# Performance work log

Hardware: AMD Instinct MI355X
Metric: run time of the kernel (lower is better)

Reference implementation:

```python
import jax, jax.numpy as jnp
import numpy as np
import math

G = 256      # graphs per batch
N0 = 256     # nodes per graph at input
RATIO = 0.5  # TopKPooling ratio


def gcn_conv(x, src, dst, ew, W, b):
    h = x @ W
    n = x.shape[0]
    deg = jnp.zeros((n,), x.dtype).at[dst].add(ew) + 1.0  # +1 for self-loop
    dinv = jax.lax.rsqrt(deg)
    norm = dinv[src] * dinv[dst] * ew
    agg = jnp.zeros_like(h).at[dst].add(norm[:, None] * h[src])
    return agg + h / deg[:, None] + b  # self-loop norm = 1/deg


def topk_pool(x, src, dst, ew, w, n_per_graph):
    # PyG TopKPooling: score = tanh(x.w/||w||); keep top ceil(ratio*n) per graph;
    # x_out = x[perm] * score[perm]; edges between dropped nodes are masked out.
    k = int(math.ceil(RATIO * n_per_graph))
    score = jnp.tanh((x @ w) / jnp.linalg.norm(w))
    top_s, top_i = jax.lax.top_k(score.reshape(G, n_per_graph), k)  # [G,k]
    perm = (top_i + (jnp.arange(G) * n_per_graph)[:, None]).reshape(-1)
    new_x = x[perm] * top_s.reshape(-1, 1)
    new_id = jnp.full((x.shape[0],), -1, jnp.int32).at[perm].set(
        jnp.arange(G * k, dtype=jnp.int32))
    ns, nd = new_id[src], new_id[dst]
    valid = (ns >= 0) & (nd >= 0)
    new_ew = ew * valid.astype(x.dtype)
    ns = jnp.where(valid, ns, 0)
    nd = jnp.where(valid, nd, 0)
    new_batch = jnp.repeat(jnp.arange(G, dtype=jnp.int32), k)
    return new_x, ns, nd, new_ew, new_batch, k


def readout(x, batch):
    # torch.cat([global_max_pool, global_mean_pool], dim=1)
    mx = jax.ops.segment_max(x, batch, num_segments=G)
    cnt = jax.ops.segment_sum(jnp.ones((x.shape[0],), x.dtype), batch, num_segments=G)
    mn = jax.ops.segment_sum(x, batch, num_segments=G) / cnt[:, None]
    return jnp.concatenate([mx, mn], axis=1)


def _forward(x, edge_index, batch, gcn_w0, gcn_b0, gcn_w1, gcn_b1, gcn_w2, gcn_b2,
             pool_w0, pool_w1, pool_w2, lin1_w, lin1_b, lin2_w, lin2_b, lin3_w, lin3_b):
    src, dst = edge_index[0], edge_index[1]
    ew = jnp.ones((src.shape[0],), x.dtype)
    npg = N0
    h = jax.nn.relu(gcn_conv(x, src, dst, ew, gcn_w0, gcn_b0))
    h, src, dst, ew, batch, npg = topk_pool(h, src, dst, ew, pool_w0, npg)
    out = readout(h, batch)
    for Wg, bg, pw in ((gcn_w1, gcn_b1, pool_w1), (gcn_w2, gcn_b2, pool_w2)):
        h = jax.nn.relu(gcn_conv(h, src, dst, ew, Wg, bg))
        h, src, dst, ew, batch, npg = topk_pool(h, src, dst, ew, pw, npg)
        out = out + readout(h, batch)
    h1 = jax.nn.relu(out @ lin1_w + lin1_b)  # dropout = identity (eval mode)
    h2 = jax.nn.relu(h1 @ lin2_w + lin2_b)
    logits = h2 @ lin3_w + lin3_b
    return jax.nn.log_softmax(logits, axis=-1)


def setup_inputs() -> dict:
    key = jax.random.key(0)
    ks = jax.random.split(key, 16)
    EPG = 2048  # edges per graph (avg degree 8)
    F_IN, H = 128, 256
    num_nodes, E = G * N0, G * EPG
    x = jax.random.normal(ks[0], (num_nodes, F_IN), jnp.float32)
    offs = jnp.repeat(jnp.arange(G, dtype=jnp.int32) * N0, EPG)
    src = offs + jax.random.randint(ks[1], (E,), 0, N0, dtype=jnp.int32)
    dst = offs + jax.random.randint(ks[2], (E,), 0, N0, dtype=jnp.int32)

    def glorot(k, shape):
        lim = float(np.sqrt(6.0 / (shape[0] + shape[1])))
        return jax.random.uniform(k, shape, jnp.float32, -lim, lim)

    return {
        "x": x,
        "edge_index": jnp.stack([src, dst]),
        "batch": jnp.arange(num_nodes, dtype=jnp.int32) // N0,
        "gcn_w0": glorot(ks[3], (F_IN, H)), "gcn_b0": jnp.zeros((H,), jnp.float32),
        "gcn_w1": glorot(ks[4], (H, H)), "gcn_b1": jnp.zeros((H,), jnp.float32),
        "gcn_w2": glorot(ks[5], (H, H)), "gcn_b2": jnp.zeros((H,), jnp.float32),
        "pool_w0": jax.random.normal(ks[6], (H,), jnp.float32) * 0.1,
        "pool_w1": jax.random.normal(ks[7], (H,), jnp.float32) * 0.1,
        "pool_w2": jax.random.normal(ks[8], (H,), jnp.float32) * 0.1,
        "lin1_w": glorot(ks[9], (2 * H, H)), "lin1_b": jnp.zeros((H,), jnp.float32),
        "lin2_w": glorot(ks[10], (H, H // 2)), "lin2_b": jnp.zeros((H // 2,), jnp.float32),
        "lin3_w": glorot(ks[11], (H // 2, 2)), "lin3_b": jnp.zeros((2,), jnp.float32),
    }


def reference(x, edge_index, batch, gcn_w0, gcn_b0, gcn_w1, gcn_b1, gcn_w2, gcn_b2,
              pool_w0, pool_w1, pool_w2, lin1_w, lin1_b, lin2_w, lin2_b, lin3_w, lin3_b):
    return _forward(x, edge_index, batch, gcn_w0, gcn_b0, gcn_w1, gcn_b1, gcn_w2, gcn_b2,
                    pool_w0, pool_w1, pool_w2, lin1_w, lin1_b, lin2_w, lin2_b, lin3_w, lin3_b)
```

## Files before the change

### kernel.cpp

```cpp
#include <hip/hip_runtime.h>
#include <hip/hip_bf16.h>
#include <math.h>

#define G_GRAPHS 256
#define EPG 2048
#define E_TOT 524288
#define HF 256
#define FIN 128

__global__ void init_cur(int* __restrict__ cur) {
    int i = blockIdx.x * blockDim.x + threadIdx.x;
    if (i < G_GRAPHS * 256) cur[i] = i & 255;
}

template <int K>
__global__ __launch_bounds__(256, 4)
void gemm_v7(const float* __restrict__ A, const float* __restrict__ W,
             float* __restrict__ C) {
    __shared__ __align__(16) float As[32 * 68];
    __shared__ __align__(16) float Wa[32 * 68];
    __shared__ __align__(16) float Wb[32 * 68];
    const int tid = threadIdx.x;
    const int tx = tid & 15;
    const int ty = tid >> 4;
    const int r0 = blockIdx.x * 64;
    const int c0 = blockIdx.y * 128;
    float acc[4][8] = {{0.f}};
    const int l8 = tid >> 3;
    const int kq = tid & 7;
    for (int k0 = 0; k0 < K; k0 += 32) {
#pragma unroll
        for (int it = 0; it < 2; ++it) {
            int row = it * 32 + l8;
            float4 v = *(const float4*)&A[(size_t)(r0 + row) * K + k0 + 4 * kq];
            int rs = row ^ (kq << 3);
            As[(4 * kq + 0) * 68 + rs] = v.x;
            As[(4 * kq + 1) * 68 + rs] = v.y;
            As[(4 * kq + 2) * 68 + rs] = v.z;
            As[(4 * kq + 3) * 68 + rs] = v.w;
        }
#pragma unroll
        for (int it = 0; it < 4; ++it) {
            int idx = it * 256 + tid;
            int kk = idx >> 5;
            int c = idx & 31;
            float4 v = *(const float4*)&W[(size_t)(k0 + kk) * 256 + c0 + 4 * c];
            if (c < 16) *(float4*)&Wa[kk * 68 + 4 * c] = v;
            else        *(float4*)&Wb[kk * 68 + 4 * (c - 16)] = v;
        }
        __syncthreads();
#pragma unroll 4
        for (int kk = 0; kk < 32; ++kk) {
            const int g = (ty * 4) ^ ((kk >> 2) << 3);
            const float4 a0 = *(const float4*)&As[kk * 68 + g];
            const float4 w0 = *(const float4*)&Wa[kk * 68 + tx * 4];
            const float4 w1 = *(const float4*)&Wb[kk * 68 + tx * 4];
            float av[4] = {a0.x, a0.y, a0.z, a0.w};
            float wv_[8] = {w0.x, w0.y, w0.z, w0.w, w1.x, w1.y, w1.z, w1.w};
#pragma unroll
            for (int i = 0; i < 4; ++i)
#pragma unroll
                for (int j = 0; j < 8; ++j)
                    acc[i][j] += av[i] * wv_[j];
        }
        __syncthreads();
    }
#pragma unroll
    for (int i = 0; i < 4; ++i) {
        float4 v0 = make_float4(acc[i][0], acc[i][1], acc[i][2], acc[i][3]);
        float4 v1 = make_float4(acc[i][4], acc[i][5], acc[i][6], acc[i][7]);
        size_t base = (size_t)(r0 + ty * 4 + i) * 256 + c0 + tx * 4;
        *(float4*)&C[base] = v0;
        *(float4*)&C[base + 64] = v1;
    }
}

__global__ __launch_bounds__(256)
void csr_build(const int* __restrict__ ei, const int* __restrict__ cur, int npg,
               int* __restrict__ degS, float* __restrict__ dinvS,
               int* __restrict__ startsS, int2* __restrict__ slots2) {
    __shared__ int cul[EPG];
    __shared__ short dstv[EPG];
    __shared__ unsigned char rnk[EPG];
    __shared__ int h[32][256];
    __shared__ int cnt[256];
    __shared__ int st[256];
    const int g = blockIdx.x;
    const int t = threadIdx.x;
    const int lane = t & 63;
    const int wv = t >> 6;

    for (int i = t; i < 32 * 256; i += 256) ((int*)h)[i] = 0;
    for (int e = t; e < EPG; e += 256) {
        size_t idx = (size_t)g * EPG + e;
        int cu = cur[g * 256 + (ei[idx] - g * 256)];
        int cv = cur[g * 256 + (ei[E_TOT + idx] - g * 256)];
        bool valid = (cu >= 0 && cv >= 0);
        cul[e] = cu;
        dstv[e] = valid ? (short)cv : (short)256;
    }
    __syncthreads();
    for (int c = wv; c < 32; c += 4) {
        int e = c * 64 + lane;
        int d = (int)dstv[e];
        unsigned long long m = ~0ULL;
#pragma unroll
        for (int b = 0; b < 9; ++b) {
            unsigned long long bb = __ballot((d >> b) & 1);
            m &= ((d >> b) & 1) ? bb : ~bb;
        }
        int r = __popcll(m & ((1ULL << lane) - 1ULL));
        rnk[e] = (unsigned char)r;
        if (r == 0 && d < 256) h[c][d] = __popcll(m);
    }
    __syncthreads();
    if (t < npg) {
        int run = 0;
        for (int c = 0; c < 32; ++c) { int v = h[c][t]; h[c][t] = run; run += v; }
        cnt[t] = run;
        degS[g * npg + t] = run + 1;
        dinvS[g * npg + t] = 1.0f / sqrtf((float)(run + 1));
    }
    __syncthreads();
    if (t == 0) {
        int run = 0;
        for (int i = 0; i < npg; ++i) { st[i] = run; run += cnt[i]; }
    }
    __syncthreads();
    if (t < npg) startsS[g * npg + t] = g * EPG + st[t];
    for (int e = t; e < EPG; e += 256) {
        int d = (int)dstv[e];
        if (d < npg) {
            int slot = st[d] + h[e >> 6][d] + (int)rnk[e];
            int cu = cul[e];
            float dv = 1.0f / sqrtf((float)(cnt[cu] + 1));
            slots2[g * EPG + slot] = make_int2(g * npg + cu, __float_as_int(dv));
        }
    }
}

__global__ __launch_bounds__(256)
void agg_score2(const int* __restrict__ degS, const float* __restrict__ dinvS,
                const int* __restrict__ startsS, const int2* __restrict__ slots2,
                const float* __restrict__ HL, float* __restrict__ H2,
                const float* __restrict__ bias, const float* __restrict__ pw,
                float* __restrict__ score, int nbOver8) {
    __shared__ float vrow[4][256];
    const int t = threadIdx.x;
    const int wv = t >> 6;
    const int lane = t & 63;
    const int blk = (blockIdx.x & 7) * nbOver8 + (blockIdx.x >> 3);
    const int node = blk * 4 + wv;
    const int cntE = degS[node] - 1;
    const float degF = (float)(cntE + 1);
    const float dn = dinvS[node];
    const int2* sl = slots2 + startsS[node];
    float ax = 0.f, ay = 0.f, az = 0.f, aw = 0.f;
    int j = 0;
    for (; j + 8 <= cntE; j += 8) {
        int2 s[8];
#pragma unroll
        for (int u = 0; u < 8; ++u) s[u] = sl[j + u];
        float4 hv[8];
#pragma unroll
        for (int u = 0; u < 8; ++u)
            hv[u] = *(const float4*)&HL[(size_t)s[u].x * 256 + 4 * lane];
#pragma unroll
        for (int u = 0; u < 8; ++u) {
            float dv = __int_as_float(s[u].y);
            ax += dv * hv[u].x; ay += dv * hv[u].y;
            az += dv * hv[u].z; aw += dv * hv[u].w;
        }
    }
    for (; j + 4 <= cntE; j += 4) {
        int2 s[4];
#pragma unroll
        for (int u = 0; u < 4; ++u) s[u] = sl[j + u];
        float4 hv[4];
#pragma unroll
        for (int u = 0; u < 4; ++u)
            hv[u] = *(const float4*)&HL[(size_t)s[u].x * 256 + 4 * lane];
#pragma unroll
        for (int u = 0; u < 4; ++u) {
            float dv = __int_as_float(s[u].y);
            ax += dv * hv[u].x; ay += dv * hv[u].y;
            az += dv * hv[u].z; aw += dv * hv[u].w;
        }
    }
    for (; j < cntE; ++j) {
        int2 sv = sl[j];
        float dv = __int_as_float(sv.y);
        float4 hv = *(const float4*)&HL[(size_t)sv.x * 256 + 4 * lane];
        ax += dv * hv.x; ay += dv * hv.y; az += dv * hv.z; aw += dv * hv.w;
    }
    const float4 hn = *(const float4*)&HL[(size_t)node * 256 + 4 * lane];
    const float4 bi = *(const float4*)&bias[4 * lane];
    float4 v;
    v.x = ax * dn + hn.x / degF + bi.x;  v.x = fmaxf(v.x, 0.f);
    v.y = ay * dn + hn.y / degF + bi.y;  v.y = fmaxf(v.y, 0.f);
    v.z = az * dn + hn.z / degF + bi.z;  v.z = fmaxf(v.z, 0.f);
    v.w = aw * dn + hn.w / degF + bi.w;  v.w = fmaxf(v.w, 0.f);
    *(float4*)&H2[(size_t)node * 256 + 4 * lane] = v;
    *(float4*)&vrow[wv][4 * lane] = v;
    float pr = 0.f, s2p = 0.f;
    for (int jj = 0; jj < 4; ++jj) {
        int f = lane + 64 * jj;
        float w = pw[f];
        pr += vrow[wv][f] * w;
        s2p += w * w;
    }
    for (int off = 32; off; off >>= 1) {
        pr += __shfl_down(pr, off, 64);
        s2p += __shfl_down(s2p, off, 64);
    }
    s2p = __shfl(s2p, 0, 64);
    if (lane == 0) score[node] = tanhf(pr / sqrtf(s2p));
}

__global__ __launch_bounds__(256)
void topk_cur(const float* __restrict__ score, int npg, int k,
              int* __restrict__ kept, int* __restrict__ cur) {
    __shared__ float ss[256];
    __shared__ int si_[256];
    __shared__ int rankOf[256];
    const int g = blockIdx.x;
    const int t = threadIdx.x;
    if (t < npg) { ss[t] = score[g * npg + t]; si_[t] = t; }
    else         { ss[t] = -INFINITY; si_[t] = 0x7FFFFFFF; }
    for (int size = 2; size <= 256; size <<= 1) {
        for (int stride = size >> 1; stride > 0; stride >>= 1) {
            __syncthreads();
            int i = t, j = t ^ stride;
            if (j > i) {
                float a = ss[i], b = ss[j];
                int ia = si_[i], ib = si_[j];
                bool inOrder = (a > b) || (a == b && ia < ib);
                bool desc = ((i & size) == 0);
                if (desc ? !inOrder : inOrder) {
                    ss[i] = b; ss[j] = a; si_[i] = ib; si_[j] = ia;
                }
            }
        }
    }
    __syncthreads();
    rankOf[t] = -1;
    __syncthreads();
    if (t < k) {
        kept[g * k + t] = g * npg + si_[t];
        rankOf[si_[t]] = t;
    }
    __syncthreads();
    {
        int v = g * 256 + t;
        int c = cur[v];
        cur[v] = (c >= 0) ? rankOf[c] : -1;
    }
}

__global__ __launch_bounds__(256)
void pool_gather(const int* __restrict__ kept, const float* __restrict__ score,
                 const float* __restrict__ H2, float* __restrict__ OUT) {
    const int j = blockIdx.x;
    const int t = threadIdx.x;
    const int o = kept[j];
    OUT[(size_t)j * 256 + t] = H2[(size_t)o * 256 + t] * score[o];
}

__global__ __launch_bounds__(256)
void readout(const float* __restrict__ X, int k, float* __restrict__ outacc,
             int first) {
    const int g = blockIdx.x;
    const int t = threadIdx.x;
    const float* base = X + (size_t)g * k * 256 + t;
    float mx = -INFINITY, sm = 0.f;
    for (int n = 0; n < k; ++n) {
        float vv = base[(size_t)n * 256];
        mx = fmaxf(mx, vv);
        sm += vv;
    }
    float mean = sm / (float)k;
    if (first) {
        outacc[g * 512 + t] = mx;
        outacc[g * 512 + 256 + t] = mean;
    } else {
        outacc[g * 512 + t] += mx;
        outacc[g * 512 + 256 + t] += mean;
    }
}

__global__ __launch_bounds__(256)
void mlp_head(const float* __restrict__ outacc,
              const float* __restrict__ l1w, const float* __restrict__ l1b,
              const float* __restrict__ l2w, const float* __restrict__ l2b,
              const float* __restrict__ l3w, const float* __restrict__ l3b,
              float* __restrict__ out) {
    __shared__ float row[512];
    __shared__ float h1[256];
    __shared__ float h2[128];
    const int g = blockIdx.x;
    const int t = threadIdx.x;
    row[t] = outacc[g * 512 + t];
    row[256 + t] = outacc[g * 512 + 256 + t];
    __syncthreads();
    {
        float a = l1b[t];
        for (int j = 0; j < 512; ++j) a += row[j] * l1w[j * 256 + t];
        h1[t] = fmaxf(a, 0.f);
    }
    __syncthreads();
    if (t < 128) {
        float a2 = l2b[t];
        for (int j = 0; j < 256; ++j) a2 += h1[j] * l2w[j * 128 + t];
        h2[t] = fmaxf(a2, 0.f);
    }
    __syncthreads();
    if (t == 0) {
        float l0 = l3b[0], l1 = l3b[1];
        for (int j = 0; j < 128; ++j) {
            float h = h2[j];
            l0 += h * l3w[j * 2 + 0];
            l1 += h * l3w[j * 2 + 1];
        }
        float m = fmaxf(l0, l1);
        float lse = m + logf(expf(l0 - m) + expf(l1 - m));
        out[g * 2 + 0] = l0 - lse;
        out[g * 2 + 1] = l1 - lse;
    }
}

__global__ __launch_bounds__(256, 1)
void gnn_mono(const float* __restrict__ x, const int* __restrict__ ei,
              const float* __restrict__ gw0, const float* __restrict__ gb0,
              const float* __restrict__ gw1, const float* __restrict__ gb1,
              const float* __restrict__ gw2, const float* __restrict__ gb2,
              const float* __restrict__ pw0, const float* __restrict__ pw1,
              const float* __restrict__ pw2,
              const float* __restrict__ l1w, const float* __restrict__ l1b,
              const float* __restrict__ l2w, const float* __restrict__ l2b,
              const float* __restrict__ l3w, const float* __restrict__ l3b,
              float* __restrict__ out, float* __restrict__ ws) {
    const int g = blockIdx.x;
    const int t = threadIdx.x;
    float* P = ws + (size_t)g * HF * 256;
    float* Q = ws + (size_t)G_GRAPHS * HF * 256 + (size_t)g * HF * 256;
    __shared__ int   eb[EPG];
    __shared__ int   slots[EPG];
    __shared__ int   curID[256];
    __shared__ int   cntL[256];
    __shared__ int   startL[256];
    __shared__ float degF[256];
    __shared__ float dinv[256];
    __shared__ float sa[256];
    __shared__ float ss[256];
    __shared__ int   si_[256];
    __shared__ float scoreV[256];
    __shared__ int   kept[128];
    __shared__ int   rankOf[256];
    __shared__ float row[512];
    for (int e = t; e < EPG; e += 256) {
        size_t idx = (size_t)g * EPG + e;
        eb[e] = ((ei[idx] - g * 256) << 8) | (ei[E_TOT + idx] - g * 256);
    }
    curID[t] = t;
    float accMx = 0.f, accMn = 0.f;
    const float* GW[3] = {gw0, gw1, gw2};
    const float* GB[3] = {gb0, gb1, gb2};
    const float* PW[3] = {pw0, pw1, pw2};
    const int kk[3] = {128, 64, 32};
    int npg = 256;
    __syncthreads();
    for (int s = 0; s < 3; ++s) {
        const int knext = kk[s];
        {
            const float* Wp = GW[s];
            const int K = (s == 0) ? FIN : HF;
            for (int n = 0; n < npg; ++n) {
                if (s == 0) { if (t < FIN) sa[t] = x[(size_t)(g * 256 + n) * FIN + t]; }
                else sa[t] = P[(size_t)n * HF + t];
                __syncthreads();
                float a = 0.f;
                for (int k2 = 0; k2 < K; ++k2) a += sa[k2] * Wp[k2 * HF + t];
                Q[(size_t)n * HF + t] = a;
                __syncthreads();
            }
        }
        cntL[t] = 0;
        __syncthreads();
        for (int e = t; e < EPG; e += 256) {
            int p = eb[e];
            int cu = curID[p >> 8], cv = curID[p & 255];
            if (cu >= 0 && cv >= 0) atomicAdd(&cntL[cv], 1);
        }
        __syncthreads();
        if (t == 0) { int run = 0; for (int i = 0; i < npg; ++i) { startL[i] = run; run += cntL[i]; } }
        __syncthreads();
        if (t < npg) {
            float d = (float)cntL[t] + 1.0f;
            degF[t] = d;
            dinv[t] = 1.0f / sqrtf(d);
            int c = startL[t];
            for (int e = 0; e < EPG; ++e) {
                int p = eb[e];
                int cu = curID[p >> 8], cv = curID[p & 255];
                if (cu >= 0 && cv >= 0 && cv == t) slots[c++] = e;
            }
        }
        __syncthreads();
        {
            const float bb = GB[s][t];
            for (int n = 0; n < npg; ++n) {
                float acc = 0.f;
                const int s0 = startL[n], s1 = s0 + cntL[n];
                for (int j = s0; j < s1; ++j) {
                    int scur = curID[eb[slots[j]] >> 8];
                    acc += dinv[scur] * Q[(size_t)scur * HF + t];
                }
                float v = acc * dinv[n] + Q[(size_t)n * HF + t] / degF[n] + bb;
                P[(size_t)n * HF + t] = fmaxf(v, 0.f);
            }
        }
        __syncthreads();
        {
            const float* pwp = PW[s];
            const int lane = t & 63, wv = t >> 6;
            float s2p = 0.f;
            for (int j = 0; j < 4; ++j) { float w = pwp[lane + 64 * j]; s2p += w * w; }
            for (int off = 32; off; off >>= 1) s2p += __shfl_down(s2p, off, 64);
            s2p = __shfl(s2p, 0, 64);
            const float nw = sqrtf(s2p);
            for (int n = wv; n < npg; n += 4) {
                float pr = 0.f;
                for (int j = 0; j < 4; ++j) { int f = lane + 64 * j; pr += P[(size_t)n * HF + f] * pwp[f]; }
                for (int off = 32; off; off >>= 1) pr += __shfl_down(pr, off, 64);
                if (lane == 0) scoreV[n] = tanhf(pr / nw);
            }
        }
        __syncthreads();
        if (t < npg) { ss[t] = scoreV[t]; si_[t] = t; }
        else         { ss[t] = -INFINITY; si_[t] = 0x7FFFFFFF; }
        for (int size = 2; size <= 256; size <<= 1) {
            for (int stride = size >> 1; stride > 0; stride >>= 1) {
                __syncthreads();
                int i = t, j = t ^ stride;
                if (j > i) {
                    float a = ss[i], b = ss[j];
                    int ia = si_[i], ib = si_[j];
                    bool inOrder = (a > b) || (a == b && ia < ib);
                    bool desc = ((i & size) == 0);
                    if (desc ? !inOrder : inOrder) { ss[i] = b; ss[j] = a; si_[i] = ib; si_[j] = ia; }
                }
            }
        }
        __syncthreads();
        if (t < knext) kept[t] = si_[t];
        __syncthreads();
        {
            float mx = -INFINITY, sm = 0.f;
            for (int n = 0; n < knext; ++n) {
                int o = kept[n];
                float vv = P[(size_t)o * HF + t] * scoreV[o];
                Q[(size_t)n * HF + t] = vv;
                mx = fmaxf(mx, vv);
                sm += vv;
            }
            accMx += mx;
            accMn += sm / (float)knext;
        }
        rankOf[t] = -1;
        __syncthreads();
        if (t < knext) rankOf[kept[t]] = t;
        __syncthreads();
        { int c = curID[t]; curID[t] = (c >= 0) ? rankOf[c] : -1; }
        __syncthreads();
        { float* tmp = P; P = Q; Q = tmp; }
        npg = knext;
    }
    row[t] = accMx;
    row[256 + t] = accMn;
    __syncthreads();
    { float a = l1b[t]; for (int j = 0; j < 512; ++j) a += row[j] * l1w[j * 256 + t]; scoreV[t] = fmaxf(a, 0.f); }
    __syncthreads();
    if (t < 128) { float a2 = l2b[t]; for (int j = 0; j < 256; ++j) a2 += scoreV[j] * l2w[j * 128 + t]; sa[t] = fmaxf(a2, 0.f); }
    __syncthreads();
    if (t == 0) {
        float l0 = l3b[0], l1 = l3b[1];
        for (int j = 0; j < 128; ++j) { float h = sa[j]; l0 += h * l3w[j * 2 + 0]; l1 += h * l3w[j * 2 + 1]; }
        float m = fmaxf(l0, l1);
        float lse = m + logf(expf(l0 - m) + expf(l1 - m));
        out[g * 2 + 0] = l0 - lse;
        out[g * 2 + 1] = l1 - lse;
    }
}

extern "C" void kernel_launch(void* const* d_in, const int* in_sizes, int n_in,
                              void* d_out, int out_size, void* d_ws, size_t ws_size,
                              hipStream_t stream) {
    const float* x   = (const float*)d_in[0];
    const int*   ei  = (const int*)d_in[1];
    const float* gw0 = (const float*)d_in[3];
    const float* gb0 = (const float*)d_in[4];
    const float* gw1 = (const float*)d_in[5];
    const float* gb1 = (const float*)d_in[6];
    const float* gw2 = (const float*)d_in[7];
    const float* gb2 = (const float*)d_in[8];
    const float* pw0 = (const float*)d_in[9];
    const float* pw1 = (const float*)d_in[10];
    const float* pw2 = (const float*)d_in[11];
    const float* l1w = (const float*)d_in[12];
    const float* l1b = (const float*)d_in[13];
    const float* l2w = (const float*)d_in[14];
    const float* l2b = (const float*)d_in[15];
    const float* l3w = (const float*)d_in[16];
    const float* l3b = (const float*)d_in[17];
    float* out = (float*)d_out;

    const size_t SLAB = (size_t)65536 * 256;
    char* p = (char*)d_ws;
    float* P      = (float*)p; p += SLAB * 4;
    float* Q      = (float*)p; p += SLAB * 4;
    int*   cur    = (int*)p;   p += (size_t)65536 * 4;
    int*   degS   = (int*)p;   p += (size_t)65536 * 4;
    float* dinvS  = (float*)p; p += (size_t)65536 * 4;
    int*   starts = (int*)p;   p += (size_t)65536 * 4;
    int2*  slots2 = (int2*)p;  p += (size_t)E_TOT * 8;
    float* score  = (float*)p; p += (size_t)65536 * 4;
    int*   kept   = (int*)p;   p += (size_t)32768 * 4;
    float* outacc = (float*)p; p += (size_t)G_GRAPHS * 512 * 4;
    const size_t needed = (size_t)(p - (char*)d_ws);

    if (ws_size < needed) {
        gnn_mono<<<G_GRAPHS, 256, 0, stream>>>(
            x, ei, gw0, gb0, gw1, gb1, gw2, gb2, pw0, pw1, pw2,
            l1w, l1b, l2w, l2b, l3w, l3b, out, (float*)d_ws);
        return;
    }

    init_cur<<<(G_GRAPHS * 256 + 255) / 256, 256, 0, stream>>>(cur);

    const int   npg[3] = {256, 128, 64};
    const int   kk[3]  = {128, 64, 32};
    const int   Ns[3]  = {65536, 32768, 16384};
    const float* GW[3] = {gw0, gw1, gw2};
    const float* GB[3] = {gb0, gb1, gb2};
    const float* PW[3] = {pw0, pw1, pw2};

    float* HLs[3]   = {P, Q, P};
    float* H2s[3]   = {Q, P, Q};
    float* POOLs[3] = {P, Q, P};

    for (int s = 0; s < 3; ++s) {
        const int n = Ns[s];
        const int k = kk[s];
        if (s == 0) {
            gemm_v7<FIN><<<dim3(n / 64, 2), 256, 0, stream>>>(x, GW[s], HLs[s]);
        } else {
            gemm_v7<HF><<<dim3(n / 64, 2), 256, 0, stream>>>(POOLs[s - 1], GW[s], HLs[s]);
        }
        csr_build<<<G_GRAPHS, 256, 0, stream>>>(ei, cur, npg[s],
                                                degS, dinvS, starts, slots2);
        agg_score2<<<n / 4, 256, 0, stream>>>(degS, dinvS, starts, slots2,
                                              HLs[s], H2s[s], GB[s], PW[s], score,
                                              n / 32);
        topk_cur<<<G_GRAPHS, 256, 0, stream>>>(score, npg[s], k, kept, cur);
        pool_gather<<<G_GRAPHS * k, 256, 0, stream>>>(kept, score, H2s[s], POOLs[s]);
        readout<<<G_GRAPHS, 256, 0, stream>>>(POOLs[s], k, outacc, s == 0 ? 1 : 0);
    }

    mlp_head<<<G_GRAPHS, 256, 0, stream>>>(outacc, l1w, l1b, l2w, l2b, l3w, l3b, out);
}
```

Before: 521.9 us.

## Fuse topk, pool gather and readout; register-prefetch next GEMM tile

The top-k kernel now gathers the kept rows scaled by their scores, writes the pooled features and computes the max and mean readout in the same block. This removes two kernel launches per stage and a re-read of the pooled matrix. Separately, the GEMM loads the next K-tile into registers before computing the current tile, so global-load latency overlaps with the FMAs, at the cost of extra registers and an extra barrier per iteration. The fused readout runs on only 256 blocks, so the gather has less parallelism than the old per-row kernel.

```diff
diff --git a/kernel.cpp b/kernel.cpp
--- a/kernel.cpp
+++ b/kernel.cpp
@@ -15,7 +15,7 @@
 
 template <int K>
 __global__ __launch_bounds__(256, 4)
-void gemm_v7(const float* __restrict__ A, const float* __restrict__ W,
+void gemm_v8(const float* __restrict__ A, const float* __restrict__ W,
              float* __restrict__ C) {
     __shared__ __align__(16) float As[32 * 68];
     __shared__ __align__(16) float Wa[32 * 68];
@@ -25,30 +25,49 @@
     const int ty = tid >> 4;
     const int r0 = blockIdx.x * 64;
     const int c0 = blockIdx.y * 128;
-    float acc[4][8] = {{0.f}};
     const int l8 = tid >> 3;
     const int kq = tid & 7;
-    for (int k0 = 0; k0 < K; k0 += 32) {
-#pragma unroll
-        for (int it = 0; it < 2; ++it) {
-            int row = it * 32 + l8;
-            float4 v = *(const float4*)&A[(size_t)(r0 + row) * K + k0 + 4 * kq];
-            int rs = row ^ (kq << 3);
-            As[(4 * kq + 0) * 68 + rs] = v.x;
-            As[(4 * kq + 1) * 68 + rs] = v.y;
-            As[(4 * kq + 2) * 68 + rs] = v.z;
-            As[(4 * kq + 3) * 68 + rs] = v.w;
-        }
-#pragma unroll
-        for (int it = 0; it < 4; ++it) {
-            int idx = it * 256 + tid;
-            int kk = idx >> 5;
-            int c = idx & 31;
-            float4 v = *(const float4*)&W[(size_t)(k0 + kk) * 256 + c0 + 4 * c];
-            if (c < 16) *(float4*)&Wa[kk * 68 + 4 * c] = v;
-            else        *(float4*)&Wb[kk * 68 + 4 * (c - 16)] = v;
-        }
-        __syncthreads();
+    const int wkk = tid >> 5;
+    const int wc = tid & 31;
+    float acc[4][8] = {{0.f}};
+    float4 va0, va1, vw0, vw1, vw2, vw3;
+
+    auto load_regs = [&](int k0) {
+        va0 = *(const float4*)&A[(size_t)(r0 + l8) * K + k0 + 4 * kq];
+        va1 = *(const float4*)&A[(size_t)(r0 + 32 + l8) * K + k0 + 4 * kq];
+        vw0 = *(const float4*)&W[(size_t)(k0 + 0  + wkk) * 256 + c0 + 4 * wc];
+        vw1 = *(const float4*)&W[(size_t)(k0 + 8  + wkk) * 256 + c0 + 4 * wc];
+        vw2 = *(const float4*)&W[(size_t)(k0 + 16 + wkk) * 256 + c0 + 4 * wc];
+        vw3 = *(const float4*)&W[(size_t)(k0 + 24 + wkk) * 256 + c0 + 4 * wc];
+    };
+    auto write_stage = [&]() {
+        {
+            int rs = l8 ^ (kq << 3);
+            As[(4 * kq + 0) * 68 + rs] = va0.x;
+            As[(4 * kq + 1) * 68 + rs] = va0.y;
+            As[(4 * kq + 2) * 68 + rs] = va0.z;
+            As[(4 * kq + 3) * 68 + rs] = va0.w;
+        }
+        {
+            int rs = (32 + l8) ^ (kq << 3);
+            As[(4 * kq + 0) * 68 + rs] = va1.x;
+            As[(4 * kq + 1) * 68 + rs] = va1.y;
+            As[(4 * kq + 2) * 68 + rs] = va1.z;
+            As[(4 * kq + 3) * 68 + rs] = va1.w;
+        }
+        if (wc < 16) {
+            *(float4*)&Wa[(0  + wkk) * 68 + 4 * wc] = vw0;
+            *(float4*)&Wa[(8  + wkk) * 68 + 4 * wc] = vw1;
+            *(float4*)&Wa[(16 + wkk) * 68 + 4 * wc] = vw2;
+            *(float4*)&Wa[(24 + wkk) * 68 + 4 * wc] = vw3;
+        } else {
+            *(float4*)&Wb[(0  + wkk) * 68 + 4 * (wc - 16)] = vw0;
+            *(float4*)&Wb[(8  + wkk) * 68 + 4 * (wc - 16)] = vw1;
+            *(float4*)&Wb[(16 + wkk) * 68 + 4 * (wc - 16)] = vw2;
+            *(float4*)&Wb[(24 + wkk) * 68 + 4 * (wc - 16)] = vw3;
+        }
+    };
+    auto compute = [&]() {
 #pragma unroll 4
         for (int kk = 0; kk < 32; ++kk) {
             const int g = (ty * 4) ^ ((kk >> 2) << 3);
@@ -63,8 +82,20 @@
                 for (int j = 0; j < 8; ++j)
                     acc[i][j] += av[i] * wv_[j];
         }
-        __syncthreads();
-    }
+    };
+
+    load_regs(0);
+    write_stage();
+    __syncthreads();
+    for (int k0 = 0; k0 < K - 32; k0 += 32) {
+        load_regs(k0 + 32);
+        compute();
+        __syncthreads();
+        write_stage();
+        __syncthreads();
+    }
+    compute();
+
 #pragma unroll
     for (int i = 0; i < 4; ++i) {
         float4 v0 = make_float4(acc[i][0], acc[i][1], acc[i][2], acc[i][3]);
@@ -218,8 +249,9 @@
 }
 
 __global__ __launch_bounds__(256)
-void topk_cur(const float* __restrict__ score, int npg, int k,
-              int* __restrict__ kept, int* __restrict__ cur) {
+void topk_fused(const float* __restrict__ score, int npg, int k,
+                const float* __restrict__ H2, float* __restrict__ OUT,
+                float* __restrict__ outacc, int* __restrict__ cur, int first) {
     __shared__ float ss[256];
     __shared__ int si_[256];
     __shared__ int rankOf[256];
@@ -245,38 +277,29 @@
     __syncthreads();
     rankOf[t] = -1;
     __syncthreads();
-    if (t < k) {
-        kept[g * k + t] = g * npg + si_[t];
-        rankOf[si_[t]] = t;
-    }
+    if (t < k) rankOf[si_[t]] = t;
     __syncthreads();
     {
         int v = g * 256 + t;
         int c = cur[v];
         cur[v] = (c >= 0) ? rankOf[c] : -1;
     }
-}
-
-__global__ __launch_bounds__(256)
-void pool_gather(const int* __restrict__ kept, const float* __restrict__ score,
-                 const float* __restrict__ H2, float* __restrict__ OUT) {
-    const int j = blockIdx.x;
-    const int t = threadIdx.x;
-    const int o = kept[j];
-    OUT[(size_t)j * 256 + t] = H2[(size_t)o * 256 + t] * score[o];
-}
-
-__global__ __launch_bounds__(256)
-void readout(const float* __restrict__ X, int k, float* __restrict__ outacc,
-             int first) {
-    const int g = blockIdx.x;
-    const int t = threadIdx.x;
-    const float* base = X + (size_t)g * k * 256 + t;
+    const size_t gb = (size_t)g * npg * 256;
     float mx = -INFINITY, sm = 0.f;
-    for (int n = 0; n < k; ++n) {
-        float vv = base[(size_t)n * 256];
-        mx = fmaxf(mx, vv);
-        sm += vv;
+    for (int n = 0; n < k; n += 4) {
+        float v0 = H2[gb + (size_t)si_[n + 0] * 256 + t] * ss[n + 0];
+        float v1 = H2[gb + (size_t)si_[n + 1] * 256 + t] * ss[n + 1];
+        float v2 = H2[gb + (size_t)si_[n + 2] * 256 + t] * ss[n + 2];
+        float v3 = H2[gb + (size_t)si_[n + 3] * 256 + t] * ss[n + 3];
+        size_t ob = ((size_t)g * k + n) * 256 + t;
+        OUT[ob]       = v0;
+        OUT[ob + 256] = v1;
+        OUT[ob + 512] = v2;
+        OUT[ob + 768] = v3;
+        mx = fmaxf(mx, v0); sm += v0;
+        mx = fmaxf(mx, v1); sm += v1;
+        mx = fmaxf(mx, v2); sm += v2;
+        mx = fmaxf(mx, v3); sm += v3;
     }
     float mean = sm / (float)k;
     if (first) {
@@ -552,18 +575,18 @@
         const int n = Ns[s];
         const int k = kk[s];
         if (s == 0) {
-            gemm_v7<FIN><<<dim3(n / 64, 2), 256, 0, stream>>>(x, GW[s], HLs[s]);
+            gemm_v8<FIN><<<dim3(n / 64, 2), 256, 0, stream>>>(x, GW[s], HLs[s]);
         } else {
-            gemm_v7<HF><<<dim3(n / 64, 2), 256, 0, stream>>>(POOLs[s - 1], GW[s], HLs[s]);
+            gemm_v8<HF><<<dim3(n / 64, 2), 256, 0, stream>>>(POOLs[s - 1], GW[s], HLs[s]);
         }
         csr_build<<<G_GRAPHS, 256, 0, stream>>>(ei, cur, npg[s],
                                                 degS, dinvS, starts, slots2);
         agg_score2<<<n / 4, 256, 0, stream>>>(degS, dinvS, starts, slots2,
                                               HLs[s], H2s[s], GB[s], PW[s], score,
                                               n / 32);
-        topk_cur<<<G_GRAPHS, 256, 0, stream>>>(score, npg[s], k, kept, cur);
-        pool_gather<<<G_GRAPHS * k, 256, 0, stream>>>(kept, score, H2s[s], POOLs[s]);
-        readout<<<G_GRAPHS, 256, 0, stream>>>(POOLs[s], k, outacc, s == 0 ? 1 : 0);
+        topk_fused<<<G_GRAPHS, 256, 0, stream>>>(score, npg[s], k,
+                                                 H2s[s], POOLs[s], outacc, cur,
+                                                 s == 0 ? 1 : 0);
     }
 
     mlp_head<<<G_GRAPHS, 256, 0, stream>>>(outacc, l1w, l1b, l2w, l2b, l3w, l3b, out);
```

Result: faster. 456.3 us (-12.6%).
